# Kernel tuning notes

Measured on AMD Instinct MI355X. Metric: run time of the kernel, lower is better.

Reference implementation:

```python
import jax, jax.numpy as jnp
import numpy as np

KEHALF = 7.199822675975274  # half Coulomb constant, eV*Angstrom/e^2
SR_CUTOFF = 4.0
LR_CUTOFF = 10.0
N_ATOMS = 262144
N_PAIRS = 16777216


def setup_inputs() -> dict:
    key = jax.random.key(0)
    k1, k2, k3, k4 = jax.random.split(key, 4)
    # distances in (0.1, 12.1) Angstrom: spans both cutoffs, avoids r=0 singularity
    Dij = jax.random.uniform(k1, (N_PAIRS,), dtype=jnp.float32) * 12.0 + 0.1
    Qa = jax.random.normal(k2, (N_ATOMS,), dtype=jnp.float32) * 0.3  # partial charges
    idx_i = jax.random.randint(k3, (N_PAIRS,), 0, N_ATOMS, dtype=jnp.int64)
    idx_j = jax.random.randint(k4, (N_PAIRS,), 0, N_ATOMS, dtype=jnp.int64)
    return {"Dij": Dij, "Qa": Qa, "idx_i": idx_i, "idx_j": idx_j}


def _poly_cutoff(r, cutoff):
    x = r / cutoff
    return jnp.where(x < 1.0, 1.0 - x * x * x * (x * (6.0 * x - 15.0) + 10.0), 0.0)


def reference(Dij, Qa, idx_i, idx_j):
    lr2 = LR_CUTOFF * LR_CUTOFF
    Qi = Qa[idx_i]                      # [P]
    Qj = Qa[idx_j]                      # [P]
    Dij_sh = jnp.sqrt(Dij * Dij + 1.0)  # shielded distance
    switch = _poly_cutoff(Dij, SR_CUTOFF / 2.0)  # phi(2r) with cutoff sr
    cswitch = 1.0 - switch
    E_ord = 1.0 / Dij + Dij / lr2 - 2.0 / LR_CUTOFF
    E_sh = 1.0 / Dij_sh + Dij_sh / lr2 - 2.0 / LR_CUTOFF
    Eele = KEHALF * Qi * Qj * (switch * E_sh + cswitch * E_ord)
    Eele = jnp.where(Dij <= LR_CUTOFF, Eele, 0.0)
    # scatter-add per-pair energies to atoms
    return jax.ops.segment_sum(Eele, idx_i, num_segments=Qa.shape[0])
```

## Files before the change

### kernel.cpp

```cpp
#include <hip/hip_runtime.h>


#define KEHALF 7.199822675975274f
#define NB    128
#define BSH   11
#define BMASK 2047
#define CAP   126976
#define CURSTRIDE 16
#define SCH   2
#define SCAP  72
#define SSTR  73
#define VSCALE 524288.0f
#define VINV   (1.0f / 524288.0f)
#define WSH   6
#define WSCALE 8192.0f
#define WSENT  (-32768)
#define P1B   512
#define P1PAIRS 8192
#define RADB  256
#define RADPAIRS 2048

__device__ __forceinline__ float radial_fast(float d) {
    float d2p1 = d * d + 1.0f;
    float rsq  = __builtin_amdgcn_rsqf(d2p1);
    float x    = 0.5f * d;
    float sw   = (x < 1.0f) ? 1.0f - x * x * x * (x * (6.0f * x - 15.0f) + 10.0f)
                            : 0.0f;
    float Eo = __builtin_amdgcn_rcpf(d) + d * 0.01f - 0.2f;
    float Es = rsq * (1.0f + 0.01f * d2p1) - 0.2f;
    return sw * Es + (1.0f - sw) * Eo;
}

__global__ __launch_bounds__(RADB) void ee_radial(
    const float* __restrict__ Dij,
    const float* __restrict__ Qa,
    const int*   __restrict__ idx_j,
    short*       __restrict__ w)
{
    long blockBase = (long)blockIdx.x * RADPAIRS;
    int tid = threadIdx.x;
#pragma unroll
    for (int g = 0; g < 2; ++g) {
        long o = blockBase + (long)(g * RADB + tid) * 4;
        int4   j4 = *reinterpret_cast<const int4*>(idx_j + o);
        float qj0 = Qa[j4.x], qj1 = Qa[j4.y], qj2 = Qa[j4.z], qj3 = Qa[j4.w];
        float4 d4 = *reinterpret_cast<const float4*>(Dij + o);
        float dd[4] = {d4.x, d4.y, d4.z, d4.w};
        float qq[4] = {qj0, qj1, qj2, qj3};
        short s[4];
#pragma unroll
        for (int k = 0; k < 4; ++k) {
            float wf = qq[k] * radial_fast(dd[k]) * WSCALE;
            wf = fminf(fmaxf(wf, -32000.0f), 32000.0f);
            int v = __float2int_rn(wf);
            s[k] = (dd[k] <= 10.0f) ? (short)v : (short)WSENT;
        }
        short4 sv = {s[0], s[1], s[2], s[3]};
        *reinterpret_cast<short4*>(w + o) = sv;
    }
}

__global__ __launch_bounds__(P1B, 4) void ee_binw(
    const short* __restrict__ w,
    const float* __restrict__ Qa,
    const int*   __restrict__ idx_i,
    unsigned int* __restrict__ list,
    unsigned int* __restrict__ gcur,
    float*        __restrict__ out)
{
    __shared__ unsigned int stage[NB * SSTR];
    __shared__ int lcur[NB + 32];
    __shared__ int gofs[NB];
    int tid = threadIdx.x;
    if (tid < NB + 32) lcur[tid] = 0;
    __syncthreads();

    long blockBase = (long)blockIdx.x * P1PAIRS;

    unsigned int EN[16];
    int          BK[16];
    int trash = NB + (tid & 31);
#pragma unroll
    for (int g = 0; g < 4; ++g) {
        long o = blockBase + (long)(g * P1B + tid) * 4;
        int4   i4 = *reinterpret_cast<const int4*>(idx_i + o);
        short4 w4 = *reinterpret_cast<const short4*>(w + o);
        short ws[4] = {w4.x, w4.y, w4.z, w4.w};
        int   ii[4] = {i4.x, i4.y, i4.z, i4.w};
#pragma unroll
        for (int k = 0; k < 4; ++k) {
            int m = g * 4 + k;
            int v = ((int)ws[k]) << WSH;
            EN[m] = ((unsigned int)(ii[k] & BMASK) << 21) |
                    ((unsigned int)v & 0x1FFFFFu);
            BK[m] = (ws[k] != WSENT) ? (ii[k] >> BSH) : trash;
        }
    }

    int SL[16];
#pragma unroll
    for (int m = 0; m < 16; ++m)
        SL[m] = atomicAdd(&lcur[BK[m]], 1);

#pragma unroll
    for (int m = 0; m < 16; ++m) {
        if (BK[m] < NB) {
            if (SL[m] < SCAP) {
                stage[BK[m] * SSTR + SL[m]] = EN[m];
            } else {
                int atom = (BK[m] << BSH) | (int)(EN[m] >> 21);
                int v    = ((int)(EN[m] << 11)) >> 11;
                atomicAdd(out + atom, KEHALF * Qa[atom] * ((float)v * VINV));
            }
        }
    }
    __syncthreads();

    if (tid < NB) {
        int n = lcur[tid];
        if (n > SCAP) n = SCAP;
        lcur[tid] = n;
        int padded = (n + 3) & ~3;
        gofs[tid] = (int)atomicAdd(&gcur[tid * CURSTRIDE], (unsigned int)padded);
    }
    __syncthreads();

    int wave = tid >> 6, lane = tid & 63;
    for (int b = wave; b < NB; b += (P1B / 64)) {
        int n = lcur[b];
        int padded = (n + 3) & ~3;
        int go = gofs[b];
        long rb = (long)b * CAP;
        for (int i = lane; i < padded; i += 64) {
            unsigned int val = (i < n) ? stage[b * SSTR + i]
                                       : ((unsigned int)(i & BMASK) << 21);
            int pos = go + i;
            if (pos < CAP)
                list[rb + pos] = val;
        }
    }
}

__global__ __launch_bounds__(P1B, 4) void ee_bin(
    const float* __restrict__ Dij,
    const float* __restrict__ Qa,
    const int*   __restrict__ idx_i,
    const int*   __restrict__ idx_j,
    unsigned int* __restrict__ list,
    unsigned int* __restrict__ gcur,
    float*        __restrict__ out)
{
    __shared__ unsigned int stage[NB * SSTR];
    __shared__ int lcur[NB + 32];
    __shared__ int gofs[NB];
    int tid = threadIdx.x;
    if (tid < NB + 32) lcur[tid] = 0;
    __syncthreads();

    long blockBase = (long)blockIdx.x * P1PAIRS;

    unsigned int EN[16];
    int          BK[16];
    int trash = NB + (tid & 31);
#pragma unroll
    for (int g = 0; g < 4; ++g) {
        long o = blockBase + ((long)(g * P1B + tid)) * 4;
        int4 j4 = *reinterpret_cast<const int4*>(idx_j + o);
        float qj0 = Qa[j4.x], qj1 = Qa[j4.y], qj2 = Qa[j4.z], qj3 = Qa[j4.w];
        float4 d4 = *reinterpret_cast<const float4*>(Dij + o);
        int4   i4 = *reinterpret_cast<const int4*>(idx_i + o);
        float dd[4] = {d4.x, d4.y, d4.z, d4.w};
        float qq[4] = {qj0, qj1, qj2, qj3};
        int   ii[4] = {i4.x, i4.y, i4.z, i4.w};
#pragma unroll
        for (int k = 0; k < 4; ++k) {
            int m = g * 4 + k;
            float d = dd[k];
            float ww = qq[k] * radial_fast(d);
            int v = __float2int_rn(ww * VSCALE);
            EN[m] = ((unsigned int)(ii[k] & BMASK) << 21) |
                    ((unsigned int)v & 0x1FFFFFu);
            BK[m] = (d <= 10.0f) ? (ii[k] >> BSH) : trash;
        }
    }

    int SL[16];
#pragma unroll
    for (int m = 0; m < 16; ++m)
        SL[m] = atomicAdd(&lcur[BK[m]], 1);

#pragma unroll
    for (int m = 0; m < 16; ++m) {
        if (BK[m] < NB) {
            if (SL[m] < SCAP) {
                stage[BK[m] * SSTR + SL[m]] = EN[m];
            } else {
                int atom = (BK[m] << BSH) | (int)(EN[m] >> 21);
                int v    = ((int)(EN[m] << 11)) >> 11;
                atomicAdd(out + atom, KEHALF * Qa[atom] * ((float)v * VINV));
            }
        }
    }
    __syncthreads();

    if (tid < NB) {
        int n = lcur[tid];
        if (n > SCAP) n = SCAP;
        lcur[tid] = n;
        int padded = (n + 3) & ~3;
        gofs[tid] = (int)atomicAdd(&gcur[tid * CURSTRIDE], (unsigned int)padded);
    }
    __syncthreads();

    int wave = tid >> 6, lane = tid & 63;
    for (int b = wave; b < NB; b += (P1B / 64)) {
        int n = lcur[b];
        int padded = (n + 3) & ~3;
        int go = gofs[b];
        long rb = (long)b * CAP;
        for (int i = lane; i < padded; i += 64) {
            unsigned int val = (i < n) ? stage[b * SSTR + i]
                                       : ((unsigned int)(i & BMASK) << 21);
            int pos = go + i;
            if (pos < CAP)
                list[rb + pos] = val;
        }
    }
}

__global__ __launch_bounds__(512) void ee_acc(
    const unsigned int* __restrict__ list,
    const unsigned int* __restrict__ gcur,
    int* __restrict__ partials)
{
    __shared__ int acc[1 << BSH];
    int b = blockIdx.x / SCH;
    int s = blockIdx.x % SCH;
    int t = threadIdx.x;
#pragma unroll
    for (int r = 0; r < (1 << BSH) / 512; ++r) acc[t + r * 512] = 0;
    __syncthreads();

    int n = (int)gcur[b * CURSTRIDE];
    if (n > CAP) n = CAP;
    int nq = n >> 2;
    int per = (nq + SCH - 1) / SCH;
    int q0 = s * per;
    int q1 = q0 + per; if (q1 > nq) q1 = nq;

    const uint4* lp4 = reinterpret_cast<const uint4*>(list + (long)b * CAP);
    for (int q = q0 + t; q < q1; q += 512) {
        uint4 u4 = lp4[q];
        unsigned int us[4] = {u4.x, u4.y, u4.z, u4.w};
#pragma unroll
        for (int k = 0; k < 4; ++k) {
            unsigned int u = us[k];
            int li = (int)(u >> 21);
            int v  = ((int)(u << 11)) >> 11;
            atomicAdd(&acc[li], v);
        }
    }
    __syncthreads();

    int* pp = partials + ((long)b * SCH + s) * (1 << BSH);
#pragma unroll
    for (int r = 0; r < (1 << BSH) / 512; ++r) pp[t + r * 512] = acc[t + r * 512];
}

__global__ __launch_bounds__(256) void ee_final(
    const int* __restrict__ partials,
    const float* __restrict__ Qa,
    float* __restrict__ out, int nAtoms)
{
    int q = blockIdx.x * blockDim.x + threadIdx.x;
    int n4 = nAtoms >> 2;
    if (q >= n4) return;
    int a0 = q << 2;
    int b  = a0 >> BSH;
    int li = a0 & BMASK;
    long base = (long)(b * SCH) * (1 << BSH) + li;
    int4 s = {0, 0, 0, 0};
#pragma unroll
    for (int r = 0; r < SCH; ++r) {
        int4 p = *reinterpret_cast<const int4*>(partials + base + (long)r * (1 << BSH));
        s.x += p.x; s.y += p.y; s.z += p.z; s.w += p.w;
    }
    float4 qv = reinterpret_cast<const float4*>(Qa)[q];
    float4 sp = reinterpret_cast<const float4*>(out)[q];
    float4 o;
    o.x = KEHALF * qv.x * ((float)s.x * VINV) + sp.x;
    o.y = KEHALF * qv.y * ((float)s.y * VINV) + sp.y;
    o.z = KEHALF * qv.z * ((float)s.z * VINV) + sp.z;
    o.w = KEHALF * qv.w * ((float)s.w * VINV) + sp.w;
    reinterpret_cast<float4*>(out)[q] = o;
}

#define FP_SCALE 4194304.0f
#define FP_INV   (1.0f / 4194304.0f)

__device__ __forceinline__ float radial_exact(float d) {
    float dsh = sqrtf(d * d + 1.0f);
    float x   = 0.5f * d;
    float sw  = (x < 1.0f) ? 1.0f - x * x * x * (x * (6.0f * x - 15.0f) + 10.0f)
                           : 0.0f;
    float Eo = 1.0f / d   + d   * 0.01f - 0.2f;
    float Es = 1.0f / dsh + dsh * 0.01f - 0.2f;
    return sw * Es + (1.0f - sw) * Eo;
}

__global__ __launch_bounds__(256) void ee_pair_fix(
    const float* __restrict__ Dij,
    const float* __restrict__ Qa,
    const int*   __restrict__ idx_i,
    const int*   __restrict__ idx_j,
    int*         __restrict__ acc,
    int P)
{
    long base = ((long)blockIdx.x * blockDim.x + threadIdx.x) * 4;
    if (base >= P) return;
    float4 d4 = *reinterpret_cast<const float4*>(Dij + base);
    int4   i4 = *reinterpret_cast<const int4*>(idx_i + base);
    int4   j4 = *reinterpret_cast<const int4*>(idx_j + base);
    float D[4]  = {d4.x, d4.y, d4.z, d4.w};
    int   ii[4] = {i4.x, i4.y, i4.z, i4.w};
    int   jj[4] = {j4.x, j4.y, j4.z, j4.w};
#pragma unroll
    for (int k = 0; k < 4; ++k) {
        float d = D[k];
        if (d > 10.0f) continue;
        float e = KEHALF * Qa[ii[k]] * Qa[jj[k]] * radial_exact(d);
        atomicAdd(acc + ii[k], __float2int_rn(e * FP_SCALE));
    }
}

__global__ __launch_bounds__(256) void ee_convert(
    const int* __restrict__ acc, float* __restrict__ out, int nAtoms)
{
    int n4 = nAtoms >> 2;
    int q = blockIdx.x * blockDim.x + threadIdx.x;
    if (q >= n4) return;
    int4 a = reinterpret_cast<const int4*>(acc)[q];
    float4 o;
    o.x = (float)a.x * FP_INV;
    o.y = (float)a.y * FP_INV;
    o.z = (float)a.z * FP_INV;
    o.w = (float)a.w * FP_INV;
    reinterpret_cast<float4*>(out)[q] = o;
}

__global__ __launch_bounds__(256) void ee_pair_direct(
    const float* __restrict__ Dij,
    const float* __restrict__ Qa,
    const int*   __restrict__ idx_i,
    const int*   __restrict__ idx_j,
    float*       __restrict__ out,
    int P)
{
    long t = (long)blockIdx.x * blockDim.x + threadIdx.x;
    if (t >= P) return;
    float d = Dij[t];
    if (d > 10.0f) return;
    atomicAdd(out + idx_i[t], KEHALF * Qa[idx_i[t]] * Qa[idx_j[t]] * radial_exact(d));
}

extern "C" void kernel_launch(void* const* d_in, const int* in_sizes, int n_in,
                              void* d_out, int out_size, void* d_ws, size_t ws_size,
                              hipStream_t stream) {
    const float* Dij   = (const float*)d_in[0];
    const float* Qa    = (const float*)d_in[1];
    const int*   idx_i = (const int*)d_in[2];
    const int*   idx_j = (const int*)d_in[3];
    float*       out   = (float*)d_out;

    int P      = in_sizes[0];
    int nAtoms = in_sizes[1];

    size_t listBytes = (size_t)NB * CAP * sizeof(unsigned int);
    size_t partBytes = (size_t)NB * SCH * (1 << BSH) * sizeof(int);
    size_t curBytes  = (size_t)NB * CURSTRIDE * sizeof(unsigned int);
    size_t wBytes    = (size_t)P * sizeof(short);
    size_t baseBytes = listBytes + partBytes + curBytes;

    if (ws_size >= baseBytes + wBytes &&
        nAtoms == NB * (1 << BSH) && (P % P1PAIRS) == 0 &&
        (P % RADPAIRS) == 0) {
        unsigned int* list = (unsigned int*)d_ws;
        int*          part = (int*)((char*)d_ws + listBytes);
        unsigned int* gcur = (unsigned int*)((char*)d_ws + listBytes + partBytes);
        short*        wbuf = (short*)((char*)d_ws + baseBytes);
        hipMemsetAsync(gcur, 0, curBytes, stream);
        hipMemsetAsync(out, 0, (size_t)out_size * sizeof(float), stream);
        ee_radial<<<P / RADPAIRS, RADB, 0, stream>>>(Dij, Qa, idx_j, wbuf);
        ee_binw<<<P / P1PAIRS, P1B, 0, stream>>>(wbuf, Qa, idx_i, list, gcur, out);
        ee_acc<<<NB * SCH, 512, 0, stream>>>(list, gcur, part);
        ee_final<<<(nAtoms / 4 + 255) / 256, 256, 0, stream>>>(part, Qa, out, nAtoms);
    } else if (ws_size >= baseBytes &&
               nAtoms == NB * (1 << BSH) && (P % P1PAIRS) == 0) {
        unsigned int* list = (unsigned int*)d_ws;
        int*          part = (int*)((char*)d_ws + listBytes);
        unsigned int* gcur = (unsigned int*)((char*)d_ws + listBytes + partBytes);
        hipMemsetAsync(gcur, 0, curBytes, stream);
        hipMemsetAsync(out, 0, (size_t)out_size * sizeof(float), stream);
        ee_bin<<<P / P1PAIRS, P1B, 0, stream>>>(Dij, Qa, idx_i, idx_j, list, gcur, out);
        ee_acc<<<NB * SCH, 512, 0, stream>>>(list, gcur, part);
        ee_final<<<(nAtoms / 4 + 255) / 256, 256, 0, stream>>>(part, Qa, out, nAtoms);
    } else if (ws_size >= (size_t)nAtoms * sizeof(int) &&
               (nAtoms & 3) == 0 && (P & 3) == 0) {
        int* acc = (int*)d_ws;
        hipMemsetAsync(acc, 0, (size_t)nAtoms * sizeof(int), stream);
        int grid = (P / 4 + 255) / 256;
        ee_pair_fix<<<grid, 256, 0, stream>>>(Dij, Qa, idx_i, idx_j, acc, P);
        ee_convert<<<(nAtoms / 4 + 255) / 256, 256, 0, stream>>>(acc, out, nAtoms);
    } else {
        hipMemsetAsync(out, 0, (size_t)out_size * sizeof(float), stream);
        int grid = (P + 255) / 256;
        ee_pair_direct<<<grid, 256, 0, stream>>>(Dij, Qa, idx_i, idx_j, out, P);
    }
}
```

Measured before the change: 312.6 us.

## Two-level binning: bin by idx_j first to localize Qa[j] gathers

Replaces the radial precompute plus i-binning with a first pass that bins pairs by idx_j's high bits, storing i, a quantized radial term and the low bits of j in split lists. A new scatter kernel then stages the 2048 charges of each j-bucket in shared memory and re-bins by idx_i into the existing list format consumed by the accumulate kernel. The aim is to turn random global Qa[j] gathers into shared-memory lookups. The cost is an extra full pass writing and reading intermediate lists, plus a coarser 14-bit quantization of the radial term.

```diff
diff --git a/kernel.cpp b/kernel.cpp
--- a/kernel.cpp
+++ b/kernel.cpp
@@ -5,20 +5,18 @@
 #define NB    128
 #define BSH   11
 #define BMASK 2047
-#define CAP   126976
+#define CAP   114688
 #define CURSTRIDE 16
 #define SCH   2
+#define SCH1  16
 #define SCAP  72
 #define SSTR  73
 #define VSCALE 524288.0f
 #define VINV   (1.0f / 524288.0f)
-#define WSH   6
-#define WSCALE 8192.0f
-#define WSENT  (-32768)
+#define RSCALE 8192.0f
+#define RINV   (1.0f / 8192.0f)
 #define P1B   512
 #define P1PAIRS 8192
-#define RADB  256
-#define RADPAIRS 2048
 
 __device__ __forceinline__ float radial_fast(float d) {
     float d2p1 = d * d + 1.0f;
@@ -31,39 +29,203 @@
     return sw * Es + (1.0f - sw) * Eo;
 }
 
-__global__ __launch_bounds__(RADB) void ee_radial(
+__global__ __launch_bounds__(P1B, 2) void ee_binj(
     const float* __restrict__ Dij,
     const float* __restrict__ Qa,
+    const int*   __restrict__ idx_i,
     const int*   __restrict__ idx_j,
-    short*       __restrict__ w)
-{
-    long blockBase = (long)blockIdx.x * RADPAIRS;
+    unsigned int*   __restrict__ l1a,
+    unsigned short* __restrict__ l1b,
+    unsigned int*   __restrict__ cur1,
+    float*          __restrict__ out)
+{
+    __shared__ unsigned int   sa[NB * SSTR];
+    __shared__ unsigned short sb[NB * SSTR];
+    __shared__ int lcur[NB + 32];
+    __shared__ int gofs[NB];
     int tid = threadIdx.x;
-#pragma unroll
-    for (int g = 0; g < 2; ++g) {
-        long o = blockBase + (long)(g * RADB + tid) * 4;
-        int4   j4 = *reinterpret_cast<const int4*>(idx_j + o);
-        float qj0 = Qa[j4.x], qj1 = Qa[j4.y], qj2 = Qa[j4.z], qj3 = Qa[j4.w];
-        float4 d4 = *reinterpret_cast<const float4*>(Dij + o);
-        float dd[4] = {d4.x, d4.y, d4.z, d4.w};
-        float qq[4] = {qj0, qj1, qj2, qj3};
-        short s[4];
+    if (tid < NB + 32) lcur[tid] = 0;
+    __syncthreads();
+
+    long blockBase = (long)blockIdx.x * P1PAIRS;
+
+    float4 d4[4]; int4 i4[4], j4[4];
+#pragma unroll
+    for (int g = 0; g < 4; ++g) {
+        long o = blockBase + (long)(g * P1B + tid) * 4;
+        d4[g] = *reinterpret_cast<const float4*>(Dij + o);
+        i4[g] = *reinterpret_cast<const int4*>(idx_i + o);
+        j4[g] = *reinterpret_cast<const int4*>(idx_j + o);
+    }
+    unsigned int   EA[16];
+    unsigned short EB[16];
+    int            BK[16];
+    int trash = NB + (tid & 31);
+#pragma unroll
+    for (int g = 0; g < 4; ++g) {
+        float dd[4] = {d4[g].x, d4[g].y, d4[g].z, d4[g].w};
+        int   ii[4] = {i4[g].x, i4[g].y, i4[g].z, i4[g].w};
+        int   jj[4] = {j4[g].x, j4[g].y, j4[g].z, j4[g].w};
 #pragma unroll
         for (int k = 0; k < 4; ++k) {
-            float wf = qq[k] * radial_fast(dd[k]) * WSCALE;
-            wf = fminf(fmaxf(wf, -32000.0f), 32000.0f);
-            int v = __float2int_rn(wf);
-            s[k] = (dd[k] <= 10.0f) ? (short)v : (short)WSENT;
-        }
-        short4 sv = {s[0], s[1], s[2], s[3]};
-        *reinterpret_cast<short4*>(w + o) = sv;
-    }
-}
-
-__global__ __launch_bounds__(P1B, 4) void ee_binw(
-    const short* __restrict__ w,
+            int m = g * 4 + k;
+            int Rq = __float2int_rn(radial_fast(dd[k]) * RSCALE);
+            EA[m] = ((unsigned int)ii[k] << 14) | ((unsigned int)Rq & 0x3FFFu);
+            EB[m] = (unsigned short)(jj[k] & BMASK);
+            BK[m] = (dd[k] <= 10.0f) ? (jj[k] >> BSH) : trash;
+        }
+    }
+
+    int SL[16];
+#pragma unroll
+    for (int m = 0; m < 16; ++m)
+        SL[m] = atomicAdd(&lcur[BK[m]], 1);
+
+#pragma unroll
+    for (int m = 0; m < 16; ++m) {
+        if (BK[m] < NB) {
+            if (SL[m] < SCAP) {
+                sa[BK[m] * SSTR + SL[m]] = EA[m];
+                sb[BK[m] * SSTR + SL[m]] = EB[m];
+            } else {
+                int atom = (int)(EA[m] >> 14);
+                int jj   = (BK[m] << BSH) | (int)EB[m];
+                int Rq   = ((int)(EA[m] << 18)) >> 18;
+                atomicAdd(out + atom,
+                          KEHALF * Qa[atom] * Qa[jj] * ((float)Rq * RINV));
+            }
+        }
+    }
+    __syncthreads();
+
+    if (tid < NB) {
+        int n = lcur[tid];
+        if (n > SCAP) n = SCAP;
+        lcur[tid] = n;
+        int padded = (n + 3) & ~3;
+        gofs[tid] = (int)atomicAdd(&cur1[tid * CURSTRIDE], (unsigned int)padded);
+    }
+    __syncthreads();
+
+    int wave = tid >> 6, lane = tid & 63;
+    for (int b = wave; b < NB; b += (P1B / 64)) {
+        int n = lcur[b];
+        int padded = (n + 3) & ~3;
+        int go = gofs[b];
+        long rb = (long)b * CAP;
+        for (int i = lane; i < padded; i += 64) {
+            bool real = (i < n);
+            unsigned int   av = real ? sa[b * SSTR + i] : 0u;
+            unsigned short bv = real ? sb[b * SSTR + i] : (unsigned short)0;
+            int pos = go + i;
+            if (pos < CAP) {
+                l1a[rb + pos] = av;
+                l1b[rb + pos] = bv;
+            } else if (real) {
+                int atom = (int)(av >> 14);
+                int jj   = (b << BSH) | (int)bv;
+                int Rq   = ((int)(av << 18)) >> 18;
+                atomicAdd(out + atom,
+                          KEHALF * Qa[atom] * Qa[jj] * ((float)Rq * RINV));
+            }
+        }
+    }
+}
+
+__global__ __launch_bounds__(512) void ee_scat(
+    const unsigned int*   __restrict__ l1a,
+    const unsigned short* __restrict__ l1b,
+    const unsigned int*   __restrict__ cur1,
+    const float*          __restrict__ Qa,
+    unsigned int* __restrict__ list2,
+    unsigned int* __restrict__ cur2,
+    float*        __restrict__ out)
+{
+    __shared__ float qs[1 << BSH];
+    __shared__ unsigned int stage[NB * SSTR];
+    __shared__ int lcur[NB + 32];
+    __shared__ int gofs[NB];
+    int b = blockIdx.x >> 4;
+    int s = blockIdx.x & 15;
+    int t = threadIdx.x;
+    if (t < NB + 32) lcur[t] = 0;
+    reinterpret_cast<float4*>(qs)[t] =
+        reinterpret_cast<const float4*>(Qa + ((long)b << BSH))[t];
+    __syncthreads();
+
+    int n1 = (int)cur1[b * CURSTRIDE];
+    if (n1 > CAP) n1 = CAP;
+    int nq = n1 >> 2;
+    int per = (nq + SCH1 - 1) >> 4;
+    int q0 = s * per;
+    int q1 = q0 + per; if (q1 > nq) q1 = nq;
+
+    const uint4* a4  = reinterpret_cast<const uint4*>(l1a + (long)b * CAP);
+    const uint2* b2p = reinterpret_cast<const uint2*>(l1b + (long)b * CAP);
+    int trash = NB + (t & 31);
+    for (int q = q0 + t; q < q1; q += 512) {
+        uint4 ua = a4[q];
+        uint2 ub = b2p[q];
+        unsigned int us[4] = {ua.x, ua.y, ua.z, ua.w};
+        int ls[4] = {(int)(ub.x & 0xFFFFu), (int)(ub.x >> 16),
+                     (int)(ub.y & 0xFFFFu), (int)(ub.y >> 16)};
+#pragma unroll
+        for (int k = 0; k < 4; ++k) {
+            unsigned int u = us[k];
+            int Rq = ((int)(u << 18)) >> 18;
+            int ii = (int)(u >> 14);
+            float vf = qs[ls[k]] * (float)Rq;
+            int v = __float2int_rn(vf * 64.0f);
+            int bk = (Rq != 0) ? (ii >> BSH) : trash;
+            int sl = atomicAdd(&lcur[bk], 1);
+            if (bk < NB) {
+                if (sl < SCAP) {
+                    stage[bk * SSTR + sl] =
+                        ((unsigned int)(ii & BMASK) << 21) |
+                        ((unsigned int)v & 0x1FFFFFu);
+                } else {
+                    atomicAdd(out + ii, KEHALF * Qa[ii] * vf * RINV);
+                }
+            }
+        }
+    }
+    __syncthreads();
+
+    if (t < NB) {
+        int n = lcur[t];
+        if (n > SCAP) n = SCAP;
+        lcur[t] = n;
+        int padded = (n + 3) & ~3;
+        gofs[t] = (int)atomicAdd(&cur2[t * CURSTRIDE], (unsigned int)padded);
+    }
+    __syncthreads();
+
+    int wave = t >> 6, lane = t & 63;
+    for (int bb = wave; bb < NB; bb += (512 / 64)) {
+        int n = lcur[bb];
+        int padded = (n + 3) & ~3;
+        int go = gofs[bb];
+        long rb = (long)bb * CAP;
+        for (int i = lane; i < padded; i += 64) {
+            unsigned int val = (i < n) ? stage[bb * SSTR + i]
+                                       : ((unsigned int)(i & BMASK) << 21);
+            int pos = go + i;
+            if (pos < CAP) {
+                list2[rb + pos] = val;
+            } else if (i < n) {
+                int atom = (bb << BSH) | (int)(val >> 21);
+                int v    = ((int)(val << 11)) >> 11;
+                atomicAdd(out + atom, KEHALF * Qa[atom] * ((float)v * VINV));
+            }
+        }
+    }
+}
+
+__global__ __launch_bounds__(P1B, 4) void ee_bin(
+    const float* __restrict__ Dij,
     const float* __restrict__ Qa,
     const int*   __restrict__ idx_i,
+    const int*   __restrict__ idx_j,
     unsigned int* __restrict__ list,
     unsigned int* __restrict__ gcur,
     float*        __restrict__ out)
@@ -82,18 +244,23 @@
     int trash = NB + (tid & 31);
 #pragma unroll
     for (int g = 0; g < 4; ++g) {
-        long o = blockBase + (long)(g * P1B + tid) * 4;
+        long o = blockBase + ((long)(g * P1B + tid)) * 4;
+        int4 j4 = *reinterpret_cast<const int4*>(idx_j + o);
+        float qj0 = Qa[j4.x], qj1 = Qa[j4.y], qj2 = Qa[j4.z], qj3 = Qa[j4.w];
+        float4 d4 = *reinterpret_cast<const float4*>(Dij + o);
         int4   i4 = *reinterpret_cast<const int4*>(idx_i + o);
-        short4 w4 = *reinterpret_cast<const short4*>(w + o);
-        short ws[4] = {w4.x, w4.y, w4.z, w4.w};
+        float dd[4] = {d4.x, d4.y, d4.z, d4.w};
+        float qq[4] = {qj0, qj1, qj2, qj3};
         int   ii[4] = {i4.x, i4.y, i4.z, i4.w};
 #pragma unroll
         for (int k = 0; k < 4; ++k) {
             int m = g * 4 + k;
-            int v = ((int)ws[k]) << WSH;
+            float d = dd[k];
+            float w = qq[k] * radial_fast(d);
+            int v = __float2int_rn(w * VSCALE);
             EN[m] = ((unsigned int)(ii[k] & BMASK) << 21) |
                     ((unsigned int)v & 0x1FFFFFu);
-            BK[m] = (ws[k] != WSENT) ? (ii[k] >> BSH) : trash;
+            BK[m] = (d <= 10.0f) ? (ii[k] >> BSH) : trash;
         }
     }
 
@@ -141,93 +308,6 @@
     }
 }
 
-__global__ __launch_bounds__(P1B, 4) void ee_bin(
-    const float* __restrict__ Dij,
-    const float* __restrict__ Qa,
-    const int*   __restrict__ idx_i,
-    const int*   __restrict__ idx_j,
-    unsigned int* __restrict__ list,
-    unsigned int* __restrict__ gcur,
-    float*        __restrict__ out)
-{
-    __shared__ unsigned int stage[NB * SSTR];
-    __shared__ int lcur[NB + 32];
-    __shared__ int gofs[NB];
-    int tid = threadIdx.x;
-    if (tid < NB + 32) lcur[tid] = 0;
-    __syncthreads();
-
-    long blockBase = (long)blockIdx.x * P1PAIRS;
-
-    unsigned int EN[16];
-    int          BK[16];
-    int trash = NB + (tid & 31);
-#pragma unroll
-    for (int g = 0; g < 4; ++g) {
-        long o = blockBase + ((long)(g * P1B + tid)) * 4;
-        int4 j4 = *reinterpret_cast<const int4*>(idx_j + o);
-        float qj0 = Qa[j4.x], qj1 = Qa[j4.y], qj2 = Qa[j4.z], qj3 = Qa[j4.w];
-        float4 d4 = *reinterpret_cast<const float4*>(Dij + o);
-        int4   i4 = *reinterpret_cast<const int4*>(idx_i + o);
-        float dd[4] = {d4.x, d4.y, d4.z, d4.w};
-        float qq[4] = {qj0, qj1, qj2, qj3};
-        int   ii[4] = {i4.x, i4.y, i4.z, i4.w};
-#pragma unroll
-        for (int k = 0; k < 4; ++k) {
-            int m = g * 4 + k;
-            float d = dd[k];
-            float ww = qq[k] * radial_fast(d);
-            int v = __float2int_rn(ww * VSCALE);
-            EN[m] = ((unsigned int)(ii[k] & BMASK) << 21) |
-                    ((unsigned int)v & 0x1FFFFFu);
-            BK[m] = (d <= 10.0f) ? (ii[k] >> BSH) : trash;
-        }
-    }
-
-    int SL[16];
-#pragma unroll
-    for (int m = 0; m < 16; ++m)
-        SL[m] = atomicAdd(&lcur[BK[m]], 1);
-
-#pragma unroll
-    for (int m = 0; m < 16; ++m) {
-        if (BK[m] < NB) {
-            if (SL[m] < SCAP) {
-                stage[BK[m] * SSTR + SL[m]] = EN[m];
-            } else {
-                int atom = (BK[m] << BSH) | (int)(EN[m] >> 21);
-                int v    = ((int)(EN[m] << 11)) >> 11;
-                atomicAdd(out + atom, KEHALF * Qa[atom] * ((float)v * VINV));
-            }
-        }
-    }
-    __syncthreads();
-
-    if (tid < NB) {
-        int n = lcur[tid];
-        if (n > SCAP) n = SCAP;
-        lcur[tid] = n;
-        int padded = (n + 3) & ~3;
-        gofs[tid] = (int)atomicAdd(&gcur[tid * CURSTRIDE], (unsigned int)padded);
-    }
-    __syncthreads();
-
-    int wave = tid >> 6, lane = tid & 63;
-    for (int b = wave; b < NB; b += (P1B / 64)) {
-        int n = lcur[b];
-        int padded = (n + 3) & ~3;
-        int go = gofs[b];
-        long rb = (long)b * CAP;
-        for (int i = lane; i < padded; i += 64) {
-            unsigned int val = (i < n) ? stage[b * SSTR + i]
-                                       : ((unsigned int)(i & BMASK) << 21);
-            int pos = go + i;
-            if (pos < CAP)
-                list[rb + pos] = val;
-        }
-    }
-}
-
 __global__ __launch_bounds__(512) void ee_acc(
     const unsigned int* __restrict__ list,
     const unsigned int* __restrict__ gcur,
@@ -375,35 +455,42 @@
     int P      = in_sizes[0];
     int nAtoms = in_sizes[1];
 
-    size_t listBytes = (size_t)NB * CAP * sizeof(unsigned int);
-    size_t partBytes = (size_t)NB * SCH * (1 << BSH) * sizeof(int);
-    size_t curBytes  = (size_t)NB * CURSTRIDE * sizeof(unsigned int);
-    size_t wBytes    = (size_t)P * sizeof(short);
-    size_t baseBytes = listBytes + partBytes + curBytes;
-
-    if (ws_size >= baseBytes + wBytes &&
-        nAtoms == NB * (1 << BSH) && (P % P1PAIRS) == 0 &&
-        (P % RADPAIRS) == 0) {
-        unsigned int* list = (unsigned int*)d_ws;
-        int*          part = (int*)((char*)d_ws + listBytes);
-        unsigned int* gcur = (unsigned int*)((char*)d_ws + listBytes + partBytes);
-        short*        wbuf = (short*)((char*)d_ws + baseBytes);
-        hipMemsetAsync(gcur, 0, curBytes, stream);
+    size_t lA    = (size_t)NB * CAP * sizeof(unsigned int);
+    size_t lB    = (size_t)NB * CAP * sizeof(unsigned short);
+    size_t l2    = (size_t)NB * CAP * sizeof(unsigned int);
+    size_t partB = (size_t)NB * SCH * (1 << BSH) * sizeof(int);
+    size_t curB  = (size_t)NB * CURSTRIDE * sizeof(unsigned int);
+    size_t splitTotal = lA + lB + l2 + partB + 2 * curB;
+
+    if (ws_size >= splitTotal && nAtoms == NB * (1 << BSH) &&
+        (P % P1PAIRS) == 0) {
+        unsigned int*   l1a  = (unsigned int*)d_ws;
+        unsigned short* l1b  = (unsigned short*)((char*)d_ws + lA);
+        unsigned int*   lst2 = (unsigned int*)((char*)d_ws + lA + lB);
+        int*            part = (int*)((char*)d_ws + lA + lB + l2);
+        unsigned int*   cur1 = (unsigned int*)((char*)d_ws + lA + lB + l2 + partB);
+        unsigned int*   cur2 = (unsigned int*)((char*)d_ws + lA + lB + l2 + partB + curB);
+        hipMemsetAsync(cur1, 0, 2 * curB, stream);
         hipMemsetAsync(out, 0, (size_t)out_size * sizeof(float), stream);
-        ee_radial<<<P / RADPAIRS, RADB, 0, stream>>>(Dij, Qa, idx_j, wbuf);
-        ee_binw<<<P / P1PAIRS, P1B, 0, stream>>>(wbuf, Qa, idx_i, list, gcur, out);
-        ee_acc<<<NB * SCH, 512, 0, stream>>>(list, gcur, part);
-        ee_final<<<(nAtoms / 4 + 255) / 256, 256, 0, stream>>>(part, Qa, out, nAtoms);
-    } else if (ws_size >= baseBytes &&
+        ee_binj<<<P / P1PAIRS, P1B, 0, stream>>>(Dij, Qa, idx_i, idx_j,
+                                                 l1a, l1b, cur1, out);
+        ee_scat<<<NB * SCH1, 512, 0, stream>>>(l1a, l1b, cur1, Qa,
+                                               lst2, cur2, out);
+        ee_acc<<<NB * SCH, 512, 0, stream>>>(lst2, cur2, part);
+        ee_final<<<(nAtoms / 4 + 255) / 256, 256, 0, stream>>>(part, Qa, out,
+                                                               nAtoms);
+    } else if (ws_size >= lA + partB + curB &&
                nAtoms == NB * (1 << BSH) && (P % P1PAIRS) == 0) {
         unsigned int* list = (unsigned int*)d_ws;
-        int*          part = (int*)((char*)d_ws + listBytes);
-        unsigned int* gcur = (unsigned int*)((char*)d_ws + listBytes + partBytes);
-        hipMemsetAsync(gcur, 0, curBytes, stream);
+        int*          part = (int*)((char*)d_ws + lA);
+        unsigned int* gcur = (unsigned int*)((char*)d_ws + lA + partB);
+        hipMemsetAsync(gcur, 0, curB, stream);
         hipMemsetAsync(out, 0, (size_t)out_size * sizeof(float), stream);
-        ee_bin<<<P / P1PAIRS, P1B, 0, stream>>>(Dij, Qa, idx_i, idx_j, list, gcur, out);
+        ee_bin<<<P / P1PAIRS, P1B, 0, stream>>>(Dij, Qa, idx_i, idx_j,
+                                                list, gcur, out);
         ee_acc<<<NB * SCH, 512, 0, stream>>>(list, gcur, part);
-        ee_final<<<(nAtoms / 4 + 255) / 256, 256, 0, stream>>>(part, Qa, out, nAtoms);
+        ee_final<<<(nAtoms / 4 + 255) / 256, 256, 0, stream>>>(part, Qa, out,
+                                                               nAtoms);
     } else if (ws_size >= (size_t)nAtoms * sizeof(int) &&
                (nAtoms & 3) == 0 && (P & 3) == 0) {
         int* acc = (int*)d_ws;
```

Result: no change. 308.8 us (-1.2%).
